# Performance work log

Hardware: AMD Instinct MI355X
Metric: run time of the kernel (lower is better)

## Reference

```python
import jax, jax.numpy as jnp
import numpy as np

ALPHA = 0.5
BETA = 0.25
D_AGG = 0.5          # delta_aggregation
D_DIS = 3.0          # delta_discrimination
OHEM_RATIO = 3.0
MAX_INST = 8         # max instance label (labels in 1..MAX_INST, 0 = background)
SMOOTH = 1e-3


def _aggr_discr(text, kernel, embed):
    # text, kernel: [HW] int32 instance labels; embed: [4, HW] float
    inst = jnp.arange(1, MAX_INST + 1)                              # [I]
    kmask = (kernel[None, :] == inst[:, None]).astype(embed.dtype)  # [I, HW]
    tmask = (text[None, :] == inst[:, None]).astype(embed.dtype)   # [I, HW]
    kcnt = kmask.sum(1)                                             # [I]
    tcnt = tmask.sum(1)
    valid = ((kcnt > 0) & (tcnt > 0)).astype(embed.dtype)           # [I]
    # per-instance kernel-mean embedding (segment mean)
    avgs = (kmask @ embed.T) / jnp.maximum(kcnt, 1.0)[:, None]      # [I, 4]
    # aggregation: per-pixel distance to the mean of its text instance
    avgs_full = jnp.concatenate([jnp.zeros((1, 4), embed.dtype), avgs], 0)  # row 0 = bg
    pix_avg = avgs_full[text]                                       # [HW, 4]
    sq = jnp.sum((embed.T - pix_avg) ** 2, axis=1)
    dist = jnp.sqrt(sq + 1e-12) - D_AGG
    lg = jnp.log1p(jnp.maximum(dist, 0.0) ** 2)                     # [HW]
    aggr_i = (tmask @ lg) / jnp.maximum(tcnt, 1.0)                  # [I]
    n = valid.sum()
    loss_aggr = jnp.where(n > 0, (aggr_i * valid).sum() / jnp.maximum(n, 1.0), 0.0)
    # discrimination: pairwise hinge between valid kernel means
    pairv = jnp.triu(valid[:, None] * valid[None, :], k=1)          # [I, I]
    sq_ij = jnp.sum((avgs[:, None, :] - avgs[None, :, :]) ** 2, axis=-1)
    d_ij = jnp.sqrt(jnp.where(pairv > 0, sq_ij, 1.0))               # safe sqrt
    L = jnp.log1p(jnp.maximum(D_DIS - d_ij, 0.0) ** 2)
    denom = n * (n - 1)
    loss_discr = jnp.where(n > 1, (L * pairv).sum() / jnp.maximum(denom, 1.0), 0.0)
    return loss_aggr, loss_discr


def _ohem(score, gt_text, gt_mask):
    # score, gt_text, gt_mask: [HW] float
    pos = gt_text > 0.5
    maskpos = gt_mask > 0.5
    pos_num = (pos & maskpos).sum()
    neg = ~pos
    neg_num = jnp.minimum((pos_num * OHEM_RATIO).astype(jnp.int32), neg.sum())
    neg_sc = jnp.where(neg, score, -jnp.inf)
    srt = -jnp.sort(-neg_sc)                                        # descending
    thr = srt[jnp.clip(neg_num - 1, 0, score.shape[0] - 1)]
    samp = ((score >= thr) | pos) & maskpos
    fallback = (pos_num == 0) | (neg_num == 0)
    return jnp.where(fallback, maskpos, samp).astype(score.dtype)


def _dice(pred_logits, target, mask):
    # all [N, HW]
    p = jax.nn.sigmoid(pred_logits) * mask
    t = (target > 0.5).astype(p.dtype) * mask
    a = jnp.sum(p * t, 1) + SMOOTH
    b = jnp.sum(p * p, 1) + SMOOTH
    c = jnp.sum(t * t, 1) + SMOOTH
    return 1.0 - 2.0 * a / (b + c)


def reference(preds, gt_texts, gt_kernels, gt_mask):
    N, C, H, W = preds.shape
    HW = H * W
    pred_text = preds[:, 0].reshape(N, HW)
    pred_kernel = preds[:, 1].reshape(N, HW)
    embed = preds[:, 2:].reshape(N, 4, HW)
    t = gt_texts.reshape(N, HW)
    k = gt_kernels.reshape(N, HW)
    m = gt_mask.reshape(N, HW).astype(preds.dtype)
    tf = t.astype(preds.dtype)
    kf = k.astype(preds.dtype)
    loss_aggr, loss_discr = jax.vmap(_aggr_discr)(t, k, embed)
    samp = jax.vmap(_ohem)(jax.lax.stop_gradient(pred_text), tf, m)
    loss_text = _dice(pred_text, tf, samp)
    samp_k = (tf > 0.5).astype(preds.dtype) * m
    loss_kernel = _dice(pred_kernel, kf, samp_k)
    # reduction='mean' then coefs [1, alpha, beta, beta]
    return jnp.stack([
        loss_text.mean(),
        ALPHA * loss_kernel.mean(),
        BETA * loss_aggr.mean(),
        BETA * loss_discr.mean(),
    ])


def setup_inputs() -> dict:
    key = jax.random.key(0)
    k1, k2, k3, k4 = jax.random.split(key, 4)
    N, H, W = 16, 512, 512
    preds = jax.random.normal(k1, (N, 6, H, W), dtype=jnp.float32)
    gt_texts = jax.random.randint(k2, (N, H, W), 0, 9, dtype=jnp.int32)
    gt_kernels = jax.random.randint(k3, (N, H, W), 0, 9, dtype=jnp.int32)
    gt_mask = jax.random.randint(k4, (N, H, W), 0, 2, dtype=jnp.int32)
    return {"preds": preds, "gt_texts": gt_texts, "gt_kernels": gt_kernels, "gt_mask": gt_mask}
```

## Files before the change

### kernel.cpp

```cpp
#include <hip/hip_runtime.h>
#include <math.h>

#define HW (512 * 512)
#define NB 16
#define NTHR 256
#define GX 256
#define REP 16

#define OFF_ACC    0
#define ACC_STRIDE (NB * 52)
#define OFF_PACC   (OFF_ACC + REP * ACC_STRIDE)
#define PACC_STRIDE (NB * 4)
#define OFF_HISTFB (OFF_PACC + REP * PACC_STRIDE)
#define OFF_NEGMX  (OFF_HISTFB + 4 * 16 * 256)
#define ZERO_WORDS (OFF_NEGMX + NB * REP)
#define OFF_TBL    ZERO_WORDS
#define OFF_THR    (OFF_TBL + 16 * 45)
#define OFF_FB     (OFF_THR + 16)
#define OFF_NVAL   (OFF_FB + 16)
#define OFF_DISCR  (OFF_NVAL + 16)
#define OFF_PREFIX (OFF_DISCR + 16)
#define OFF_KKC    (OFF_PREFIX + 16)
#define OFF_NEGC   (OFF_KKC + 16)
#define OFF_CNTS   (OFF_NEGC + 16)
#define OFF_KEYS   (OFF_CNTS + NB * 1024)
#define WS_FULL_BYTES ((size_t)(OFF_KEYS + NB * HW) * 4)


__device__ __forceinline__ unsigned fmap(float f) {
    unsigned u = __float_as_uint(f);
    return (u & 0x80000000u) ? ~u : (u | 0x80000000u);
}
__device__ __forceinline__ float funmap(unsigned u) {
    return (u & 0x80000000u) ? __uint_as_float(u & 0x7FFFFFFFu)
                             : __uint_as_float(~u);
}
__device__ __forceinline__ float wred(float x) {
#pragma unroll
    for (int o = 32; o; o >>= 1) x += __shfl_xor(x, o);
    return x;
}
__device__ __forceinline__ unsigned wredu(unsigned x) {
#pragma unroll
    for (int o = 32; o; o >>= 1) x += __shfl_xor(x, o);
    return x;
}
__device__ __forceinline__ unsigned wredumax(unsigned x) {
#pragma unroll
    for (int o = 32; o; o >>= 1) x = max(x, (unsigned)__shfl_xor((int)x, o));
    return x;
}

__global__ __launch_bounds__(NTHR, 2) void k_stats(const float* __restrict__ preds,
                        const int* __restrict__ text,
                        const int* __restrict__ kern,
                        const int* __restrict__ mask,
                        unsigned* __restrict__ wsu, int do_compact) {
    float* wsf = (float*)wsu;
    const int b = blockIdx.y;
    const int tid = threadIdx.x;
    const int lane = tid & 63;
    const unsigned long long lmask = (1ull << lane) - 1ull;
    __shared__ float sacc[52];
    if (tid < 52) sacc[tid] = 0.f;
    __syncthreads();

    const int base = blockIdx.x * (NTHR * 4) + tid * 4;
    const int* tb = text + b * HW;
    const int* kb = kern + b * HW;
    const int* mb = mask + b * HW;
    const float* p0 = preds + (size_t)(b * 6 + 0) * HW;
    const float* p1 = preds + (size_t)(b * 6 + 1) * HW;
    const float* e0 = preds + (size_t)(b * 6 + 2) * HW;
    const float* e1 = e0 + HW;
    const float* e2 = e0 + 2 * HW;
    const float* e3 = e0 + 3 * HW;

    const int4 t4 = *(const int4*)(tb + base);
    const int4 k4 = *(const int4*)(kb + base);
    const int4 m4 = *(const int4*)(mb + base);
    const float4 s4 = *(const float4*)(p0 + base);
    const float4 q4 = *(const float4*)(p1 + base);
    const float4 a4 = *(const float4*)(e0 + base);
    const float4 b4 = *(const float4*)(e1 + base);
    const float4 c4 = *(const float4*)(e2 + base);
    const float4 d4 = *(const float4*)(e3 + base);

    float ks[32];
#pragma unroll
    for (int i = 0; i < 32; i++) ks[i] = 0.f;
    float r_ak = 0.f, r_bk = 0.f, r_ck = 0.f;
    unsigned kcW[8] = {0, 0, 0, 0, 0, 0, 0, 0};
    unsigned tcW[8] = {0, 0, 0, 0, 0, 0, 0, 0};
    unsigned posW = 0;

#define PIX(T, K, M, Q, A, B, C, D) do {                                     \
        bool pos_ = (T) > 0, mp_ = (M) > 0;                                  \
        float sm_ = (pos_ && mp_) ? 1.f : 0.f;                               \
        float sg_ = 1.f / (1.f + expf(-(Q)));                                \
        float ik_ = ((K) > 0) ? 1.f : 0.f;                                   \
        r_ak += sm_ * sg_ * ik_;                                             \
        r_bk += sm_ * sg_ * sg_;                                             \
        r_ck += sm_ * ik_;                                                   \
        posW += (unsigned)__popcll(__ballot(pos_ && mp_));                   \
        _Pragma("unroll")                                                    \
        for (int i_ = 0; i_ < 8; i_++) {                                     \
            bool hit_ = ((K) == i_ + 1);                                     \
            kcW[i_] += (unsigned)__popcll(__ballot(hit_));                   \
            tcW[i_] += (unsigned)__popcll(__ballot((T) == i_ + 1));          \
            float h_ = hit_ ? 1.f : 0.f;                                     \
            ks[i_ * 4 + 0] += h_ * (A);                                      \
            ks[i_ * 4 + 1] += h_ * (B);                                      \
            ks[i_ * 4 + 2] += h_ * (C);                                      \
            ks[i_ * 4 + 3] += h_ * (D);                                      \
        }                                                                    \
    } while (0)

    PIX(t4.x, k4.x, m4.x, q4.x, a4.x, b4.x, c4.x, d4.x);
    PIX(t4.y, k4.y, m4.y, q4.y, a4.y, b4.y, c4.y, d4.y);
    PIX(t4.z, k4.z, m4.z, q4.z, a4.z, b4.z, c4.z, d4.z);
    PIX(t4.w, k4.w, m4.w, q4.w, a4.w, b4.w, c4.w, d4.w);
#undef PIX

    const unsigned long long m0 = __ballot(t4.x == 0);
    const unsigned long long m1 = __ballot(t4.y == 0);
    const unsigned long long m2 = __ballot(t4.z == 0);
    const unsigned long long m3 = __ballot(t4.w == 0);
    const unsigned c0 = (unsigned)__popcll(m0), c1 = (unsigned)__popcll(m1);
    const unsigned c2 = (unsigned)__popcll(m2), c3 = (unsigned)__popcll(m3);
    const unsigned tot = c0 + c1 + c2 + c3;
    const int seg = blockIdx.x * 4 + (tid >> 6);
    if (lane == 0) wsu[OFF_CNTS + b * 1024 + seg] = tot;
    if (do_compact) {
        unsigned* keys = wsu + OFF_KEYS + (size_t)b * HW + (size_t)seg * 256;
        if (t4.x == 0) keys[(unsigned)__popcll(m0 & lmask)] = fmap(s4.x);
        if (t4.y == 0) keys[c0 + (unsigned)__popcll(m1 & lmask)] = fmap(s4.y);
        if (t4.z == 0) keys[c0 + c1 + (unsigned)__popcll(m2 & lmask)] = fmap(s4.z);
        if (t4.w == 0) keys[c0 + c1 + c2 + (unsigned)__popcll(m3 & lmask)] = fmap(s4.w);
    }
    {
        unsigned mk = 0u;
        if (t4.x == 0) mk = max(mk, ~fmap(s4.x));
        if (t4.y == 0) mk = max(mk, ~fmap(s4.y));
        if (t4.z == 0) mk = max(mk, ~fmap(s4.z));
        if (t4.w == 0) mk = max(mk, ~fmap(s4.w));
        mk = wredumax(mk);
        if (lane == 0 && mk)
            atomicMax(&wsu[OFF_NEGMX + b * REP + (blockIdx.x & (REP - 1))], mk);
    }

#pragma unroll
    for (int i = 0; i < 32; i++) {
        float v = wred(ks[i]);
        if (lane == 0) atomicAdd(&sacc[16 + i], v);
    }
    {
        float v = wred(r_ak); if (lane == 0) atomicAdd(&sacc[49], v);
        v = wred(r_bk); if (lane == 0) atomicAdd(&sacc[50], v);
        v = wred(r_ck); if (lane == 0) atomicAdd(&sacc[51], v);
    }
    if (lane == 0) {
#pragma unroll
        for (int i = 0; i < 8; i++) {
            atomicAdd(&sacc[i], (float)kcW[i]);
            atomicAdd(&sacc[8 + i], (float)tcW[i]);
        }
        atomicAdd(&sacc[48], (float)posW);
    }
    __syncthreads();
    if (tid < 52) {
        const int rep = blockIdx.x & (REP - 1);
        atomicAdd(&wsf[OFF_ACC + rep * ACC_STRIDE + b * 52 + tid], sacc[tid]);
    }
}

__global__ void k_sel(unsigned* __restrict__ wsu, int do_select) {
    float* wsf = (float*)wsu;
    const int b = blockIdx.x;
    const int tid = threadIdx.x;
    const int lane = tid & 63;
    __shared__ float s_acc[52];
    __shared__ float s_avg[8][4];
    __shared__ int s_valid[8];
    __shared__ unsigned s_hist[256];
    __shared__ unsigned s_negtot;
    __shared__ unsigned s_kk, s_prefix;

    if (tid < 52) {
        float v = 0.f;
#pragma unroll
        for (int r = 0; r < REP; r++) v += wsf[OFF_ACC + r * ACC_STRIDE + b * 52 + tid];
        s_acc[tid] = v;
    }
    if (tid == 0) s_negtot = 0u;
    __syncthreads();

    const unsigned myc = wsu[OFF_CNTS + b * 1024 + tid];
    {
        unsigned cw = wredu(myc);
        if (lane == 0) atomicAdd(&s_negtot, cw);
    }
    if (tid < 8) {
        float kcf = s_acc[tid];
        float tcf = s_acc[8 + tid];
        int valid = (kcf > 0.f && tcf > 0.f) ? 1 : 0;
        float inv = 1.f / fmaxf(kcf, 1.f);
        float w = valid ? 1.f / fmaxf(tcf, 1.f) : 0.f;
#pragma unroll
        for (int c = 0; c < 4; c++) {
            float a = s_acc[16 + tid * 4 + c] * inv;
            s_avg[tid][c] = a;
            wsf[OFF_TBL + b * 45 + (tid + 1) * 5 + c] = a;
        }
        s_valid[tid] = valid;
        wsf[OFF_TBL + b * 45 + (tid + 1) * 5 + 4] = w;
    }
    if (tid >= 8 && tid < 13) wsf[OFF_TBL + b * 45 + (tid - 8)] = 0.f;
    __syncthreads();
    if (tid == 0) {
        int nval = 0;
        for (int i = 0; i < 8; i++) nval += s_valid[i];
        float L = 0.f;
        for (int i = 0; i < 8; i++)
            for (int j = i + 1; j < 8; j++)
                if (s_valid[i] && s_valid[j]) {
                    float sq = 0.f;
                    for (int c = 0; c < 4; c++) {
                        float d = s_avg[i][c] - s_avg[j][c];
                        sq += d * d;
                    }
                    float h = fmaxf(3.0f - sqrtf(sq), 0.f);
                    L += log1pf(h * h);
                }
        wsf[OFF_DISCR + b] = (nval > 1) ? L / fmaxf((float)(nval * (nval - 1)), 1.f) : 0.f;
        wsu[OFF_NVAL + b] = (unsigned)nval;
        unsigned pos = (unsigned)s_acc[48];
        unsigned neg = s_negtot;
        wsu[OFF_NEGC + b] = neg;
        unsigned nn = min(pos * 3u, neg);
        int fb = (pos == 0u || nn == 0u) ? 1 : 0;
        wsu[OFF_FB + b] = (unsigned)fb;
        wsu[OFF_KKC + b] = fb ? 0u : nn;
        wsu[OFF_PREFIX + b] = 0u;
        wsf[OFF_THR + b] = 0.f;
        unsigned kk = fb ? 0u : nn;
        if (!fb && nn == neg) {
            unsigned mx = 0u;
#pragma unroll
            for (int r = 0; r < REP; r++) mx = max(mx, wsu[OFF_NEGMX + b * REP + r]);
            wsf[OFF_THR + b] = funmap(~mx);
            kk = 0u;
        }
        s_kk = kk;
        s_prefix = 0u;
    }
    __syncthreads();
    if (!do_select) return;
    if (s_kk == 0u) return;
    const unsigned* keys = wsu + OFF_KEYS + (size_t)b * HW + (size_t)tid * 256;
    unsigned prefix = 0u;
    for (int pass = 0; pass < 4; pass++) {
        const int shift = 24 - 8 * pass;
        const unsigned fmask = (pass == 0) ? 0u : (0xFFFFFFFFu << (shift + 8));
        if (tid < 256) s_hist[tid] = 0u;
        __syncthreads();
        for (unsigned i = 0; i < myc; i++) {
            unsigned key = keys[i];
            if ((key & fmask) == prefix) atomicAdd(&s_hist[(key >> shift) & 255u], 1u);
        }
        __syncthreads();
        if (tid == 0) {
            unsigned k2 = s_kk;
            for (int bin = 255; bin >= 0; --bin) {
                unsigned c = s_hist[bin];
                if (k2 <= c) { s_prefix = prefix | (((unsigned)bin) << shift); s_kk = k2; break; }
                k2 -= c;
            }
        }
        __syncthreads();
        prefix = s_prefix;
    }
    if (tid == 0) wsf[OFF_THR + b] = funmap(prefix);
}

__global__ void k_hist(const float* __restrict__ preds, const int* __restrict__ text,
                       unsigned* __restrict__ wsu, int pass) {
    const int b = blockIdx.y;
    const int tid = threadIdx.x;
    __shared__ unsigned h[256];
    h[tid] = 0u;
    __syncthreads();
    const unsigned prefix = wsu[OFF_PREFIX + b];
    const int shift = 24 - 8 * pass;
    const unsigned fmask = (pass == 0) ? 0u : (0xFFFFFFFFu << (shift + 8));
    const int* tb = text + b * HW;
    const float* pt = preds + (size_t)(b * 6) * HW;
    for (int p = blockIdx.x * NTHR + tid; p < HW; p += gridDim.x * NTHR) {
        if (tb[p] == 0) {
            unsigned key = fmap(pt[p]);
            if ((key & fmask) == prefix) atomicAdd(&h[(key >> shift) & 255u], 1u);
        }
    }
    __syncthreads();
    if (h[tid]) atomicAdd(&wsu[OFF_HISTFB + pass * 4096 + b * 256 + tid], h[tid]);
}
__global__ void k_select(unsigned* __restrict__ wsu, int pass) {
    int b = threadIdx.x;
    if (b >= NB) return;
    float* wsf = (float*)wsu;
    unsigned k = wsu[OFF_KKC + b];
    unsigned prefix = wsu[OFF_PREFIX + b];
    const int shift = 24 - 8 * pass;
    const unsigned* h = &wsu[OFF_HISTFB + pass * 4096 + b * 256];
    if (k > 0) {
        for (int bin = 255; bin >= 0; --bin) {
            unsigned c = h[bin];
            if (k <= c) { prefix |= ((unsigned)bin) << shift; break; }
            k -= c;
        }
        wsu[OFF_KKC + b] = k;
        wsu[OFF_PREFIX + b] = prefix;
    }
    if (pass == 3) wsf[OFF_THR + b] = funmap(prefix);
}

__global__ __launch_bounds__(NTHR, 2) void k_pix(const float* __restrict__ preds,
                      const int* __restrict__ text,
                      const int* __restrict__ mask,
                      unsigned* __restrict__ wsu) {
    float* wsf = (float*)wsu;
    const int b = blockIdx.y;
    const int tid = threadIdx.x;
    const int lane = tid & 63;
    __shared__ float stbl[45];
    __shared__ float sred[4];
    __shared__ float sthr;
    __shared__ unsigned sfb;
    if (tid < 45) stbl[tid] = wsf[OFF_TBL + b * 45 + tid];
    if (tid < 4) sred[tid] = 0.f;
    if (tid == 0) { sthr = wsf[OFF_THR + b]; sfb = wsu[OFF_FB + b]; }
    __syncthreads();
    const float thr = sthr;
    const bool fb = sfb != 0u;
    float r_at = 0.f, r_bt = 0.f, r_ct = 0.f, r_ag = 0.f;
    const int base = blockIdx.x * (NTHR * 4) + tid * 4;
    const int* tb = text + b * HW;
    const int* mb = mask + b * HW;
    const float* p0 = preds + (size_t)(b * 6) * HW;
    const float* e0 = preds + (size_t)(b * 6 + 2) * HW;
    const float* e1 = e0 + HW;
    const float* e2 = e0 + 2 * HW;
    const float* e3 = e0 + 3 * HW;
    const int4 t4 = *(const int4*)(tb + base);
    const int4 m4 = *(const int4*)(mb + base);
    const float4 s4 = *(const float4*)(p0 + base);
    const float4 a4 = *(const float4*)(e0 + base);
    const float4 b4 = *(const float4*)(e1 + base);
    const float4 c4 = *(const float4*)(e2 + base);
    const float4 d4 = *(const float4*)(e3 + base);

#define PPIX(T, M, S, A, B, C, D) do {                                       \
        bool pos_ = (T) > 0;                                                 \
        bool samp_ = fb ? ((M) > 0) : ((((S) >= thr) || pos_) && ((M) > 0)); \
        float sg_ = 1.f / (1.f + expf(-(S)));                                \
        float smf_ = samp_ ? 1.f : 0.f;                                      \
        float it_ = pos_ ? 1.f : 0.f;                                        \
        r_at += smf_ * sg_ * it_;                                            \
        r_bt += smf_ * sg_ * sg_;                                            \
        r_ct += smf_ * it_;                                                  \
        int t5_ = min((T), 8) * 5;                                           \
        float d0_ = (A) - stbl[t5_ + 0];                                     \
        float d1_ = (B) - stbl[t5_ + 1];                                     \
        float d2_ = (C) - stbl[t5_ + 2];                                     \
        float d3_ = (D) - stbl[t5_ + 3];                                     \
        float w_ = stbl[t5_ + 4];                                            \
        float sq_ = d0_ * d0_ + d1_ * d1_ + d2_ * d2_ + d3_ * d3_;           \
        float dist_ = sqrtf(sq_ + 1e-12f) - 0.5f;                            \
        float hp_ = fmaxf(dist_, 0.f);                                       \
        r_ag += w_ * log1pf(hp_ * hp_);                                      \
    } while (0)

    PPIX(t4.x, m4.x, s4.x, a4.x, b4.x, c4.x, d4.x);
    PPIX(t4.y, m4.y, s4.y, a4.y, b4.y, c4.y, d4.y);
    PPIX(t4.z, m4.z, s4.z, a4.z, b4.z, c4.z, d4.z);
    PPIX(t4.w, m4.w, s4.w, a4.w, b4.w, c4.w, d4.w);
#undef PPIX

    {
        float v = wred(r_at); if (lane == 0) atomicAdd(&sred[0], v);
        v = wred(r_bt); if (lane == 0) atomicAdd(&sred[1], v);
        v = wred(r_ct); if (lane == 0) atomicAdd(&sred[2], v);
        v = wred(r_ag); if (lane == 0) atomicAdd(&sred[3], v);
    }
    __syncthreads();
    if (tid < 4) {
        const int rep = blockIdx.x & (REP - 1);
        atomicAdd(&wsf[OFF_PACC + rep * PACC_STRIDE + b * 4 + tid], sred[tid]);
    }
}

__global__ void k_final(unsigned* __restrict__ wsu, float* __restrict__ out) {
    float* wsf = (float*)wsu;
    __shared__ float lt[NB], lk[NB], la[NB], ld[NB];
    int b = threadIdx.x;
    if (b < NB) {
        const float S = 1e-3f;
        float ak = 0.f, bk = 0.f, ck = 0.f, at = 0.f, bt = 0.f, ct = 0.f, ag = 0.f;
#pragma unroll
        for (int r = 0; r < REP; r++) {
            ak += wsf[OFF_ACC + r * ACC_STRIDE + b * 52 + 49];
            bk += wsf[OFF_ACC + r * ACC_STRIDE + b * 52 + 50];
            ck += wsf[OFF_ACC + r * ACC_STRIDE + b * 52 + 51];
            at += wsf[OFF_PACC + r * PACC_STRIDE + b * 4 + 0];
            bt += wsf[OFF_PACC + r * PACC_STRIDE + b * 4 + 1];
            ct += wsf[OFF_PACC + r * PACC_STRIDE + b * 4 + 2];
            ag += wsf[OFF_PACC + r * PACC_STRIDE + b * 4 + 3];
        }
        lt[b] = 1.f - 2.f * (at + S) / ((bt + S) + (ct + S));
        lk[b] = 1.f - 2.f * (ak + S) / ((bk + S) + (ck + S));
        int nval = (int)wsu[OFF_NVAL + b];
        la[b] = (nval > 0) ? ag / fmaxf((float)nval, 1.f) : 0.f;
        ld[b] = wsf[OFF_DISCR + b];
    }
    __syncthreads();
    if (b == 0) {
        float st = 0, sk = 0, sa = 0, sd = 0;
        for (int i = 0; i < NB; i++) { st += lt[i]; sk += lk[i]; sa += la[i]; sd += ld[i]; }
        out[0] = st / NB;
        out[1] = 0.5f * sk / NB;
        out[2] = 0.25f * sa / NB;
        out[3] = 0.25f * sd / NB;
    }
}

extern "C" void kernel_launch(void* const* d_in, const int* in_sizes, int n_in,
                              void* d_out, int out_size, void* d_ws, size_t ws_size,
                              hipStream_t stream) {
    const float* preds = (const float*)d_in[0];
    const int* text = (const int*)d_in[1];
    const int* kern = (const int*)d_in[2];
    const int* mask = (const int*)d_in[3];
    unsigned* wsu = (unsigned*)d_ws;
    float* out = (float*)d_out;

    const int do_compact = (ws_size >= WS_FULL_BYTES) ? 1 : 0;

    hipMemsetAsync(d_ws, 0, (size_t)ZERO_WORDS * 4, stream);

    dim3 grid(GX, NB);
    k_stats<<<grid, NTHR, 0, stream>>>(preds, text, kern, mask, wsu, do_compact);
    k_sel<<<NB, 1024, 0, stream>>>(wsu, do_compact);
    if (!do_compact) {
        dim3 hgrid(128, NB);
        for (int pass = 0; pass < 4; pass++) {
            k_hist<<<hgrid, NTHR, 0, stream>>>(preds, text, wsu, pass);
            k_select<<<1, 64, 0, stream>>>(wsu, pass);
        }
    }
    k_pix<<<grid, NTHR, 0, stream>>>(preds, text, mask, wsu);
    k_final<<<1, 64, 0, stream>>>(wsu, out);
}
```

Measured before the change: 260.3 us.

## Process four chunks per thread and shrink segment count for selection

k_stats and k_pix now loop over four 1024-pixel chunks per block, with a quarter as many blocks. Per-thread partial sums are reduced and atomically flushed once per block instead of once per chunk, which cuts reduction and atomic overhead. Compaction segments grow to 1024 keys, so there are 256 segments per image and k_sel runs with 256 threads, each scanning a longer segment during its radix passes. This trades fewer atomics and reductions for fewer resident blocks and longer serial scans per thread in k_sel.

```diff
diff --git a/kernel.cpp b/kernel.cpp
--- a/kernel.cpp
+++ b/kernel.cpp
@@ -4,7 +4,10 @@
 #define HW (512 * 512)
 #define NB 16
 #define NTHR 256
-#define GX 256
+#define GXS 64
+#define CH 4
+#define NSEG 256
+#define SEGSZ 1024
 #define REP 16
 
 #define OFF_ACC    0
@@ -23,7 +26,7 @@
 #define OFF_KKC    (OFF_PREFIX + 16)
 #define OFF_NEGC   (OFF_KKC + 16)
 #define OFF_CNTS   (OFF_NEGC + 16)
-#define OFF_KEYS   (OFF_CNTS + NB * 1024)
+#define OFF_KEYS   (OFF_CNTS + NB * NSEG)
 #define WS_FULL_BYTES ((size_t)(OFF_KEYS + NB * HW) * 4)
 
 
@@ -65,7 +68,6 @@
     if (tid < 52) sacc[tid] = 0.f;
     __syncthreads();
 
-    const int base = blockIdx.x * (NTHR * 4) + tid * 4;
     const int* tb = text + b * HW;
     const int* kb = kern + b * HW;
     const int* mb = mask + b * HW;
@@ -76,15 +78,10 @@
     const float* e2 = e0 + 2 * HW;
     const float* e3 = e0 + 3 * HW;
 
-    const int4 t4 = *(const int4*)(tb + base);
-    const int4 k4 = *(const int4*)(kb + base);
-    const int4 m4 = *(const int4*)(mb + base);
-    const float4 s4 = *(const float4*)(p0 + base);
-    const float4 q4 = *(const float4*)(p1 + base);
-    const float4 a4 = *(const float4*)(e0 + base);
-    const float4 b4 = *(const float4*)(e1 + base);
-    const float4 c4 = *(const float4*)(e2 + base);
-    const float4 d4 = *(const float4*)(e3 + base);
+    const int seg = blockIdx.x * 4 + (tid >> 6);
+    unsigned* keys = wsu + OFF_KEYS + (size_t)b * HW + (size_t)seg * SEGSZ;
+    unsigned segoff = 0;
+    unsigned mkAll = 0u;
 
     float ks[32];
 #pragma unroll
@@ -93,6 +90,19 @@
     unsigned kcW[8] = {0, 0, 0, 0, 0, 0, 0, 0};
     unsigned tcW[8] = {0, 0, 0, 0, 0, 0, 0, 0};
     unsigned posW = 0;
+
+#pragma unroll 1
+    for (int c = 0; c < CH; c++) {
+        const int base = blockIdx.x * (NTHR * 4 * CH) + c * (NTHR * 4) + tid * 4;
+        const int4 t4 = *(const int4*)(tb + base);
+        const int4 k4 = *(const int4*)(kb + base);
+        const int4 m4 = *(const int4*)(mb + base);
+        const float4 s4 = *(const float4*)(p0 + base);
+        const float4 q4 = *(const float4*)(p1 + base);
+        const float4 a4 = *(const float4*)(e0 + base);
+        const float4 b4 = *(const float4*)(e1 + base);
+        const float4 c4 = *(const float4*)(e2 + base);
+        const float4 d4 = *(const float4*)(e3 + base);
 
 #define PIX(T, K, M, Q, A, B, C, D) do {                                     \
         bool pos_ = (T) > 0, mp_ = (M) > 0;                                  \
@@ -116,38 +126,37 @@
         }                                                                    \
     } while (0)
 
-    PIX(t4.x, k4.x, m4.x, q4.x, a4.x, b4.x, c4.x, d4.x);
-    PIX(t4.y, k4.y, m4.y, q4.y, a4.y, b4.y, c4.y, d4.y);
-    PIX(t4.z, k4.z, m4.z, q4.z, a4.z, b4.z, c4.z, d4.z);
-    PIX(t4.w, k4.w, m4.w, q4.w, a4.w, b4.w, c4.w, d4.w);
+        PIX(t4.x, k4.x, m4.x, q4.x, a4.x, b4.x, c4.x, d4.x);
+        PIX(t4.y, k4.y, m4.y, q4.y, a4.y, b4.y, c4.y, d4.y);
+        PIX(t4.z, k4.z, m4.z, q4.z, a4.z, b4.z, c4.z, d4.z);
+        PIX(t4.w, k4.w, m4.w, q4.w, a4.w, b4.w, c4.w, d4.w);
 #undef PIX
 
-    const unsigned long long m0 = __ballot(t4.x == 0);
-    const unsigned long long m1 = __ballot(t4.y == 0);
-    const unsigned long long m2 = __ballot(t4.z == 0);
-    const unsigned long long m3 = __ballot(t4.w == 0);
-    const unsigned c0 = (unsigned)__popcll(m0), c1 = (unsigned)__popcll(m1);
-    const unsigned c2 = (unsigned)__popcll(m2), c3 = (unsigned)__popcll(m3);
-    const unsigned tot = c0 + c1 + c2 + c3;
-    const int seg = blockIdx.x * 4 + (tid >> 6);
-    if (lane == 0) wsu[OFF_CNTS + b * 1024 + seg] = tot;
-    if (do_compact) {
-        unsigned* keys = wsu + OFF_KEYS + (size_t)b * HW + (size_t)seg * 256;
-        if (t4.x == 0) keys[(unsigned)__popcll(m0 & lmask)] = fmap(s4.x);
-        if (t4.y == 0) keys[c0 + (unsigned)__popcll(m1 & lmask)] = fmap(s4.y);
-        if (t4.z == 0) keys[c0 + c1 + (unsigned)__popcll(m2 & lmask)] = fmap(s4.z);
-        if (t4.w == 0) keys[c0 + c1 + c2 + (unsigned)__popcll(m3 & lmask)] = fmap(s4.w);
-    }
-    {
+        const unsigned long long m0 = __ballot(t4.x == 0);
+        const unsigned long long m1 = __ballot(t4.y == 0);
+        const unsigned long long m2 = __ballot(t4.z == 0);
+        const unsigned long long m3 = __ballot(t4.w == 0);
+        const unsigned c0 = (unsigned)__popcll(m0), c1 = (unsigned)__popcll(m1);
+        const unsigned c2 = (unsigned)__popcll(m2), c3 = (unsigned)__popcll(m3);
+        if (do_compact) {
+            if (t4.x == 0) keys[segoff + (unsigned)__popcll(m0 & lmask)] = fmap(s4.x);
+            if (t4.y == 0) keys[segoff + c0 + (unsigned)__popcll(m1 & lmask)] = fmap(s4.y);
+            if (t4.z == 0) keys[segoff + c0 + c1 + (unsigned)__popcll(m2 & lmask)] = fmap(s4.z);
+            if (t4.w == 0) keys[segoff + c0 + c1 + c2 + (unsigned)__popcll(m3 & lmask)] = fmap(s4.w);
+        }
+        segoff += c0 + c1 + c2 + c3;
         unsigned mk = 0u;
         if (t4.x == 0) mk = max(mk, ~fmap(s4.x));
         if (t4.y == 0) mk = max(mk, ~fmap(s4.y));
         if (t4.z == 0) mk = max(mk, ~fmap(s4.z));
         if (t4.w == 0) mk = max(mk, ~fmap(s4.w));
-        mk = wredumax(mk);
-        if (lane == 0 && mk)
-            atomicMax(&wsu[OFF_NEGMX + b * REP + (blockIdx.x & (REP - 1))], mk);
-    }
+        mkAll = max(mkAll, mk);
+    }
+
+    if (lane == 0) wsu[OFF_CNTS + b * NSEG + seg] = segoff;
+    mkAll = wredumax(mkAll);
+    if (lane == 0 && mkAll)
+        atomicMax(&wsu[OFF_NEGMX + b * REP + (blockIdx.x & (REP - 1))], mkAll);
 
 #pragma unroll
     for (int i = 0; i < 32; i++) {
@@ -195,7 +204,7 @@
     if (tid == 0) s_negtot = 0u;
     __syncthreads();
 
-    const unsigned myc = wsu[OFF_CNTS + b * 1024 + tid];
+    const unsigned myc = wsu[OFF_CNTS + b * NSEG + tid];
     {
         unsigned cw = wredu(myc);
         if (lane == 0) atomicAdd(&s_negtot, cw);
@@ -257,12 +266,12 @@
     __syncthreads();
     if (!do_select) return;
     if (s_kk == 0u) return;
-    const unsigned* keys = wsu + OFF_KEYS + (size_t)b * HW + (size_t)tid * 256;
+    const unsigned* keys = wsu + OFF_KEYS + (size_t)b * HW + (size_t)tid * SEGSZ;
     unsigned prefix = 0u;
     for (int pass = 0; pass < 4; pass++) {
         const int shift = 24 - 8 * pass;
         const unsigned fmask = (pass == 0) ? 0u : (0xFFFFFFFFu << (shift + 8));
-        if (tid < 256) s_hist[tid] = 0u;
+        s_hist[tid] = 0u;
         __syncthreads();
         for (unsigned i = 0; i < myc; i++) {
             unsigned key = keys[i];
@@ -343,7 +352,6 @@
     const float thr = sthr;
     const bool fb = sfb != 0u;
     float r_at = 0.f, r_bt = 0.f, r_ct = 0.f, r_ag = 0.f;
-    const int base = blockIdx.x * (NTHR * 4) + tid * 4;
     const int* tb = text + b * HW;
     const int* mb = mask + b * HW;
     const float* p0 = preds + (size_t)(b * 6) * HW;
@@ -351,13 +359,17 @@
     const float* e1 = e0 + HW;
     const float* e2 = e0 + 2 * HW;
     const float* e3 = e0 + 3 * HW;
-    const int4 t4 = *(const int4*)(tb + base);
-    const int4 m4 = *(const int4*)(mb + base);
-    const float4 s4 = *(const float4*)(p0 + base);
-    const float4 a4 = *(const float4*)(e0 + base);
-    const float4 b4 = *(const float4*)(e1 + base);
-    const float4 c4 = *(const float4*)(e2 + base);
-    const float4 d4 = *(const float4*)(e3 + base);
+
+#pragma unroll 1
+    for (int c = 0; c < CH; c++) {
+        const int base = blockIdx.x * (NTHR * 4 * CH) + c * (NTHR * 4) + tid * 4;
+        const int4 t4 = *(const int4*)(tb + base);
+        const int4 m4 = *(const int4*)(mb + base);
+        const float4 s4 = *(const float4*)(p0 + base);
+        const float4 a4 = *(const float4*)(e0 + base);
+        const float4 b4 = *(const float4*)(e1 + base);
+        const float4 c4 = *(const float4*)(e2 + base);
+        const float4 d4 = *(const float4*)(e3 + base);
 
 #define PPIX(T, M, S, A, B, C, D) do {                                       \
         bool pos_ = (T) > 0;                                                 \
@@ -380,11 +392,12 @@
         r_ag += w_ * log1pf(hp_ * hp_);                                      \
     } while (0)
 
-    PPIX(t4.x, m4.x, s4.x, a4.x, b4.x, c4.x, d4.x);
-    PPIX(t4.y, m4.y, s4.y, a4.y, b4.y, c4.y, d4.y);
-    PPIX(t4.z, m4.z, s4.z, a4.z, b4.z, c4.z, d4.z);
-    PPIX(t4.w, m4.w, s4.w, a4.w, b4.w, c4.w, d4.w);
+        PPIX(t4.x, m4.x, s4.x, a4.x, b4.x, c4.x, d4.x);
+        PPIX(t4.y, m4.y, s4.y, a4.y, b4.y, c4.y, d4.y);
+        PPIX(t4.z, m4.z, s4.z, a4.z, b4.z, c4.z, d4.z);
+        PPIX(t4.w, m4.w, s4.w, a4.w, b4.w, c4.w, d4.w);
 #undef PPIX
+    }
 
     {
         float v = wred(r_at); if (lane == 0) atomicAdd(&sred[0], v);
@@ -447,9 +460,9 @@
 
     hipMemsetAsync(d_ws, 0, (size_t)ZERO_WORDS * 4, stream);
 
-    dim3 grid(GX, NB);
+    dim3 grid(GXS, NB);
     k_stats<<<grid, NTHR, 0, stream>>>(preds, text, kern, mask, wsu, do_compact);
-    k_sel<<<NB, 1024, 0, stream>>>(wsu, do_compact);
+    k_sel<<<NB, NTHR, 0, stream>>>(wsu, do_compact);
     if (!do_compact) {
         dim3 hgrid(128, NB);
         for (int pass = 0; pass < 4; pass++) {
```

New measurement: 243.7 us. -6.4%, faster.
